# Kernel optimization log

Hardware: AMD Instinct MI355X
Metric: run time of the kernel (lower is better)

Reference implementation:

```python
import jax, jax.numpy as jnp
import numpy as np

SEQ, D_IN, D_OUT = 4096, 1024, 1024


def setup_inputs() -> dict:
    key = jax.random.key(0)
    kx, kq, kk, kv = jax.random.split(key, 4)
    x = jax.random.normal(kx, (SEQ, D_IN), dtype=jnp.float32)
    # original uses torch.rand (uniform [0,1)) for parameter init
    W_query = jax.random.uniform(kq, (D_IN, D_OUT), dtype=jnp.float32)
    W_key = jax.random.uniform(kk, (D_IN, D_OUT), dtype=jnp.float32)
    W_value = jax.random.uniform(kv, (D_IN, D_OUT), dtype=jnp.float32)
    return {"x": x, "W_query": W_query, "W_key": W_key, "W_value": W_value}


def reference(x, W_query, W_key, W_value):
    queries = x @ W_query          # [S, d_out]
    keys = x @ W_key               # [S, d_out]
    values = x @ W_value           # [S, d_out]
    scale = keys.shape[-1] ** 0.5
    attn_scores = queries @ keys.T # [S, S]
    attn_weights = jax.nn.softmax(attn_scores / scale, axis=-1)
    context_vec = attn_weights @ values  # [S, d_out]
    return context_vec
```

## Files before the change

### kernel.cpp

```cpp
#include <hip/hip_runtime.h>
#include <stdint.h>

#define SEQ 4096
#define DM 1024

typedef __attribute__((ext_vector_type(8))) short short8;
typedef __attribute__((ext_vector_type(4))) float f32x4;
typedef __attribute__((ext_vector_type(16))) float f32x16;
typedef unsigned short ushort_t;

__device__ inline ushort_t f2bf(float f) {
  union { float f; uint32_t u; } v; v.f = f;
  return (ushort_t)((v.u + 0x7FFFu + ((v.u >> 16) & 1u)) >> 16);
}
__device__ inline float bf2f(ushort_t h) {
  union { uint32_t u; float f; } v; v.u = ((uint32_t)h) << 16;
  return v.f;
}

__device__ inline void async_copy16(const void* g, void* lds) {
  __builtin_amdgcn_global_load_lds(
      (const __attribute__((address_space(1))) uint32_t*)g,
      (__attribute__((address_space(3))) uint32_t*)lds, 16, 0, 0);
}


__global__ __launch_bounds__(256, 3)
void gemm_qkv(const ushort_t* __restrict__ A, const ushort_t* __restrict__ Bt,
              ushort_t* __restrict__ Qb, ushort_t* __restrict__ Kb,
              ushort_t* __restrict__ Vb) {
  __shared__ ushort_t As[2][128 * 32];
  __shared__ ushort_t Bs[2][128 * 32];
  const int t = threadIdx.x;
  const int wave = t >> 6, lane = t & 63;
  const int quad = lane >> 4, l16 = lane & 15;
  const int m0 = blockIdx.y * 128, n0 = blockIdx.x * 128;
  const int wm = (wave & 1) * 64, wn = (wave >> 1) * 64;

  f32x4 acc[4][4] = {};

  if (n0 >= 2048) {
    ushort_t* Af = &As[0][0];
    ushort_t* Bf = &Bs[0][0];
    const int srow8 = lane >> 3;
    const int gcol8 = (((lane & 7) - srow8) & 7) * 8;
    const int rs = l16 & 7;
    for (int k0 = 0; k0 < 1024; k0 += 64) {
#pragma unroll
      for (int i = 0; i < 4; ++i) {
        int c = wave * 4 + i;
        async_copy16(A + (size_t)(m0 + c * 8 + srow8) * 2048 + k0 + gcol8,
                     Af + c * 512);
        async_copy16(Bt + (size_t)(n0 + c * 8 + srow8) * 2048 + k0 + gcol8,
                     Bf + c * 512);
      }
      __syncthreads();
#pragma unroll
      for (int q = 0; q < 2; ++q) {
        short8 a[4], b[4];
#pragma unroll
        for (int i = 0; i < 4; ++i) {
          int slot = ((q * 4 + quad + rs) & 7) * 8;
          a[i] = *(const short8*)(Af + (wm + i * 16 + l16) * 64 + slot);
          b[i] = *(const short8*)(Bf + (wn + i * 16 + l16) * 64 + slot);
        }
#pragma unroll
        for (int i = 0; i < 4; ++i)
#pragma unroll
          for (int j = 0; j < 4; ++j)
            acc[i][j] = __builtin_amdgcn_mfma_f32_16x16x32_bf16(a[i], b[j], acc[i][j], 0, 0, 0);
      }
      __syncthreads();
    }
    const int cb = n0 - 2048;
#pragma unroll
    for (int i = 0; i < 4; ++i)
#pragma unroll
      for (int j = 0; j < 4; ++j)
#pragma unroll
        for (int r = 0; r < 4; ++r) {
          int row = m0 + wm + i * 16 + quad * 4 + r;
          int col = cb + wn + j * 16 + l16;
          Vb[(size_t)row * 1024 + col] = f2bf(acc[i][j][r]);
        }
    return;
  }

  const int srow = lane >> 2;
  const int sf = (srow >> 1) & 3;
  const int gcol = (((lane & 3) - sf) & 3) * 8;
  const int rf = (l16 >> 1) & 3;
  const int aslot = ((quad + rf) & 3) * 8;

  for (int k0 = 0; k0 < 1024; k0 += 32) {
#pragma unroll
    for (int i = 0; i < 2; ++i) {
      int c = wave * 2 + i;
      const ushort_t* ga = A + (size_t)(m0 + c * 16 + srow) * 2048 + k0 + gcol;
      const ushort_t* gb = Bt + (size_t)(n0 + c * 16 + srow) * 2048 + k0 + gcol;
      async_copy16(ga,        As[0] + c * 512);
      async_copy16(ga + 1024, As[1] + c * 512);
      async_copy16(gb,        Bs[0] + c * 512);
      async_copy16(gb + 1024, Bs[1] + c * 512);
    }
    __syncthreads();
    short8 a[4], b[4], x[4];
#pragma unroll
    for (int i = 0; i < 4; ++i) {
      a[i] = *(const short8*)(As[0] + (wm + i * 16 + l16) * 32 + aslot);
      b[i] = *(const short8*)(Bs[0] + (wn + i * 16 + l16) * 32 + aslot);
    }
#pragma unroll
    for (int i = 0; i < 4; ++i)
#pragma unroll
      for (int j = 0; j < 4; ++j)
        acc[i][j] = __builtin_amdgcn_mfma_f32_16x16x32_bf16(a[i], b[j], acc[i][j], 0, 0, 0);
#pragma unroll
    for (int j = 0; j < 4; ++j)
      x[j] = *(const short8*)(Bs[1] + (wn + j * 16 + l16) * 32 + aslot);
#pragma unroll
    for (int i = 0; i < 4; ++i)
#pragma unroll
      for (int j = 0; j < 4; ++j)
        acc[i][j] = __builtin_amdgcn_mfma_f32_16x16x32_bf16(a[i], x[j], acc[i][j], 0, 0, 0);
#pragma unroll
    for (int i = 0; i < 4; ++i)
      x[i] = *(const short8*)(As[1] + (wm + i * 16 + l16) * 32 + aslot);
#pragma unroll
    for (int i = 0; i < 4; ++i)
#pragma unroll
      for (int j = 0; j < 4; ++j)
        acc[i][j] = __builtin_amdgcn_mfma_f32_16x16x32_bf16(x[i], b[j], acc[i][j], 0, 0, 0);
    __syncthreads();
  }

  ushort_t* Cm = (n0 < 1024) ? Qb : Kb;
  const int cb = n0 & 1023;
#pragma unroll
  for (int i = 0; i < 4; ++i)
#pragma unroll
    for (int j = 0; j < 4; ++j)
#pragma unroll
      for (int r = 0; r < 4; ++r) {
        int row = m0 + wm + i * 16 + quad * 4 + r;
        int col = cb + wn + j * 16 + l16;
        float v = acc[i][j][r];
        ushort_t h = f2bf(v);
        size_t base = (size_t)row * 2048 + col;
        Cm[base] = h;
        Cm[base + 1024] = f2bf(v - bf2f(h));
      }
}

__global__ __launch_bounds__(256, 4)
void gemm_sc(const ushort_t* __restrict__ A, const ushort_t* __restrict__ Bt,
             float* __restrict__ C, float scale) {
  const int m0 = blockIdx.y * 128, n0 = blockIdx.x * 128;

  __shared__ ushort_t As[2][128 * 32];
  __shared__ ushort_t Bs[2][128 * 32];
  const int t = threadIdx.x;
  const int wave = t >> 6, lane = t & 63;
  const int quad = lane >> 4, l16 = lane & 15;
  const int wm = (wave & 1) * 64, wn = (wave >> 1) * 64;
  const int srow = lane >> 2;
  const int sf = (srow >> 1) & 3;
  const int gcol = (((lane & 3) - sf) & 3) * 8;
  const int rf = (l16 >> 1) & 3;
  const int aslot = ((quad + rf) & 3) * 8;

  f32x4 acc[4][4] = {};

  for (int k0 = 0; k0 < 1024; k0 += 32) {
#pragma unroll
    for (int i = 0; i < 2; ++i) {
      int c = wave * 2 + i;
      const ushort_t* ga = A + (size_t)(m0 + c * 16 + srow) * 2048 + k0 + gcol;
      const ushort_t* gb = Bt + (size_t)(n0 + c * 16 + srow) * 2048 + k0 + gcol;
      async_copy16(ga,        As[0] + c * 512);
      async_copy16(ga + 1024, As[1] + c * 512);
      async_copy16(gb,        Bs[0] + c * 512);
      async_copy16(gb + 1024, Bs[1] + c * 512);
    }
    __syncthreads();
    short8 a[4], b[4], x[4];
#pragma unroll
    for (int i = 0; i < 4; ++i) {
      a[i] = *(const short8*)(As[0] + (wm + i * 16 + l16) * 32 + aslot);
      b[i] = *(const short8*)(Bs[0] + (wn + i * 16 + l16) * 32 + aslot);
    }
#pragma unroll
    for (int i = 0; i < 4; ++i)
#pragma unroll
      for (int j = 0; j < 4; ++j)
        acc[i][j] = __builtin_amdgcn_mfma_f32_16x16x32_bf16(a[i], b[j], acc[i][j], 0, 0, 0);
#pragma unroll
    for (int j = 0; j < 4; ++j)
      x[j] = *(const short8*)(Bs[1] + (wn + j * 16 + l16) * 32 + aslot);
#pragma unroll
    for (int i = 0; i < 4; ++i)
#pragma unroll
      for (int j = 0; j < 4; ++j)
        acc[i][j] = __builtin_amdgcn_mfma_f32_16x16x32_bf16(a[i], x[j], acc[i][j], 0, 0, 0);
#pragma unroll
    for (int i = 0; i < 4; ++i)
      x[i] = *(const short8*)(As[1] + (wm + i * 16 + l16) * 32 + aslot);
#pragma unroll
    for (int i = 0; i < 4; ++i)
#pragma unroll
      for (int j = 0; j < 4; ++j)
        acc[i][j] = __builtin_amdgcn_mfma_f32_16x16x32_bf16(x[i], b[j], acc[i][j], 0, 0, 0);
    __syncthreads();
  }

#pragma unroll
  for (int i = 0; i < 4; ++i)
#pragma unroll
    for (int j = 0; j < 4; ++j)
#pragma unroll
      for (int r = 0; r < 4; ++r) {
        int row = m0 + wm + i * 16 + quad * 4 + r;
        int col = n0 + wn + j * 16 + l16;
        C[(size_t)row * SEQ + col] = acc[i][j][r] * scale;
      }
}

__global__ __launch_bounds__(256)
void gemm_pv(const ushort_t* __restrict__ P, const ushort_t* __restrict__ Vt,
             float* __restrict__ Obuf) {
  const int id = blockIdx.x;
  const int g = ((id >> 6) << 3) | (id & 7);
  const int jt = (id >> 3) & 7;
  const int z = g & 3, m = g >> 2;
  const int m0 = m * 128, n0 = jt * 128, kbeg = z * 1024;
  float* Ob = Obuf + (size_t)z * SEQ * DM;

  __shared__ ushort_t As[128 * 64];
  __shared__ ushort_t Bs[128 * 64];
  const int t = threadIdx.x;
  const int wave = t >> 6, lane = t & 63;
  const int l32 = lane & 31, khalf = lane >> 5;
  const int wm = (wave & 1) * 64, wn = (wave >> 1) * 64;
  const int srow = lane >> 3;
  const int gcol = (((lane & 7) - srow) & 7) * 8;
  const int rrot = lane & 7;

  f32x16 acc[2][2] = {};
  for (int k0 = kbeg; k0 < kbeg + 1024; k0 += 64) {
#pragma unroll
    for (int i = 0; i < 4; ++i) {
      int c = wave * 4 + i;
      async_copy16(P + (size_t)(m0 + c * 8 + srow) * 4096 + k0 + gcol,
                   As + c * 512);
      async_copy16(Vt + (size_t)(n0 + c * 8 + srow) * SEQ + k0 + gcol,
                   Bs + c * 512);
    }
    __syncthreads();
#pragma unroll
    for (int q = 0; q < 4; ++q) {
      const int slot = ((q * 2 + khalf + rrot) & 7) * 8;
      short8 a[2], b[2];
#pragma unroll
      for (int i = 0; i < 2; ++i) {
        a[i] = *(const short8*)(As + (wm + i * 32 + l32) * 64 + slot);
        b[i] = *(const short8*)(Bs + (wn + i * 32 + l32) * 64 + slot);
      }
#pragma unroll
      for (int i = 0; i < 2; ++i)
#pragma unroll
        for (int j = 0; j < 2; ++j)
          acc[i][j] = __builtin_amdgcn_mfma_f32_32x32x16_bf16(a[i], b[j], acc[i][j], 0, 0, 0);
    }
    __syncthreads();
  }
#pragma unroll
  for (int i = 0; i < 2; ++i)
#pragma unroll
    for (int j = 0; j < 2; ++j)
#pragma unroll
      for (int r = 0; r < 16; ++r) {
        int row = m0 + wm + i * 32 + (r & 3) + 8 * (r >> 2) + 4 * khalf;
        int col = n0 + wn + j * 32 + l32;
        Ob[(size_t)row * DM + col] = acc[i][j][r];
      }
}

__global__ __launch_bounds__(256)
void reduce4(const float* __restrict__ B, float* __restrict__ out) {
  const size_t i = ((size_t)blockIdx.x * 256 + threadIdx.x) * 4;
  const size_t n = (size_t)SEQ * DM;
  float4 s0 = *(const float4*)(B + i);
  float4 s1 = *(const float4*)(B + n + i);
  float4 s2 = *(const float4*)(B + 2 * n + i);
  float4 s3 = *(const float4*)(B + 3 * n + i);
  float4 o;
  o.x = s0.x + s1.x + s2.x + s3.x;
  o.y = s0.y + s1.y + s2.y + s3.y;
  o.z = s0.z + s1.z + s2.z + s3.z;
  o.w = s0.w + s1.w + s2.w + s3.w;
  *(float4*)(out + i) = o;
}

__global__ __launch_bounds__(256)
void split_x(const float* __restrict__ x, ushort_t* __restrict__ Xp) {
  int idx = (blockIdx.x * 256 + threadIdx.x) * 4;
  int r = idx >> 10, c = idx & 1023;
  float4 v = *(const float4*)(x + idx);
  ushort4 hi, lo;
  hi.x = f2bf(v.x); lo.x = f2bf(v.x - bf2f(hi.x));
  hi.y = f2bf(v.y); lo.y = f2bf(v.y - bf2f(hi.y));
  hi.z = f2bf(v.z); lo.z = f2bf(v.z - bf2f(hi.z));
  hi.w = f2bf(v.w); lo.w = f2bf(v.w - bf2f(hi.w));
  *(ushort4*)(Xp + (size_t)r * 2048 + c) = hi;
  *(ushort4*)(Xp + (size_t)r * 2048 + 1024 + c) = lo;
}

__global__ __launch_bounds__(256)
void splitT_w3(const float* __restrict__ W0, const float* __restrict__ W1,
               const float* __restrict__ W2, ushort_t* __restrict__ Wp) {
  const float* W = (blockIdx.z == 0) ? W0 : (blockIdx.z == 1) ? W1 : W2;
  ushort_t* Wo = Wp + (size_t)blockIdx.z * DM * 2048;
  __shared__ float tile[64][65];
  const int bn = blockIdx.x * 64, bk = blockIdx.y * 64;
  const int tx = threadIdx.x & 63, ty = threadIdx.x >> 6;
#pragma unroll
  for (int i = ty; i < 64; i += 4)
    tile[i][tx] = W[(size_t)(bk + i) * DM + bn + tx];
  __syncthreads();
#pragma unroll
  for (int i = ty; i < 64; i += 4) {
    float v = tile[tx][i];
    ushort_t h = f2bf(v);
    Wo[(size_t)(bn + i) * 2048 + bk + tx] = h;
    Wo[(size_t)(bn + i) * 2048 + 1024 + bk + tx] = f2bf(v - bf2f(h));
  }
}

__global__ __launch_bounds__(256)
void transpose_bf16(const ushort_t* __restrict__ in, int istride,
                    ushort_t* __restrict__ out, int R) {
  __shared__ ushort_t tile[64][65];
  const int bc = blockIdx.x * 64, br = blockIdx.y * 64;
  const int tx = threadIdx.x & 63, ty = threadIdx.x >> 6;
#pragma unroll
  for (int i = ty; i < 64; i += 4)
    tile[i][tx] = in[(size_t)(br + i) * istride + bc + tx];
  __syncthreads();
#pragma unroll
  for (int i = ty; i < 64; i += 4)
    out[(size_t)(bc + i) * R + br + tx] = tile[tx][i];
}

__global__ __launch_bounds__(256)
void softmax_rows(const float* __restrict__ S, ushort_t* __restrict__ Pd) {
  const int row = blockIdx.x;
  const int t = threadIdx.x, lane = t & 63, wave = t >> 6;
  const float4* s4 = (const float4*)(S + (size_t)row * SEQ);
  float4 v[4];
  float m = -3.4e38f;
#pragma unroll
  for (int i = 0; i < 4; ++i) {
    v[i] = s4[i * 256 + t];
    m = fmaxf(m, fmaxf(fmaxf(v[i].x, v[i].y), fmaxf(v[i].z, v[i].w)));
  }
  __shared__ float redm[4], reds[4];
#pragma unroll
  for (int o = 32; o; o >>= 1) m = fmaxf(m, __shfl_xor(m, o));
  if (lane == 0) redm[wave] = m;
  __syncthreads();
  m = fmaxf(fmaxf(redm[0], redm[1]), fmaxf(redm[2], redm[3]));
  float sum = 0.f;
#pragma unroll
  for (int i = 0; i < 4; ++i) {
    v[i].x = __expf(v[i].x - m); v[i].y = __expf(v[i].y - m);
    v[i].z = __expf(v[i].z - m); v[i].w = __expf(v[i].w - m);
    sum += v[i].x + v[i].y + v[i].z + v[i].w;
  }
#pragma unroll
  for (int o = 32; o; o >>= 1) sum += __shfl_xor(sum, o);
  if (lane == 0) reds[wave] = sum;
  __syncthreads();
  const float inv = 1.f / (reds[0] + reds[1] + reds[2] + reds[3]);
  ushort4* p4 = (ushort4*)(Pd + (size_t)row * SEQ);
#pragma unroll
  for (int i = 0; i < 4; ++i) {
    ushort4 o;
    o.x = f2bf(v[i].x * inv); o.y = f2bf(v[i].y * inv);
    o.z = f2bf(v[i].z * inv); o.w = f2bf(v[i].w * inv);
    p4[i * 256 + t] = o;
  }
}

extern "C" void kernel_launch(void* const* d_in, const int* in_sizes, int n_in,
                              void* d_out, int out_size, void* d_ws, size_t ws_size,
                              hipStream_t stream) {
  const float* x  = (const float*)d_in[0];
  const float* Wq = (const float*)d_in[1];
  const float* Wk = (const float*)d_in[2];
  const float* Wv = (const float*)d_in[3];
  float* out = (float*)d_out;
  char* ws = (char*)d_ws;
  const size_t MB = (size_t)1 << 20;
  ushort_t* Xp   = (ushort_t*)(ws + 0 * MB);
  ushort_t* Wall = (ushort_t*)(ws + 16 * MB);
  ushort_t* Qb   = (ushort_t*)(ws + 28 * MB);
  ushort_t* Kb   = (ushort_t*)(ws + 44 * MB);
  ushort_t* Vb   = (ushort_t*)(ws + 60 * MB);
  ushort_t* VT   = (ushort_t*)(ws + 68 * MB);
  float*    S    = (float*)(ws + 76 * MB);
  ushort_t* Pd   = (ushort_t*)(ws + 0 * MB);
  float*    Obuf = (float*)(ws + 76 * MB);

  split_x<<<SEQ * DM / 1024, 256, 0, stream>>>(x, Xp);
  splitT_w3<<<dim3(16, 16, 3), 256, 0, stream>>>(Wq, Wk, Wv, Wall);

  gemm_qkv<<<dim3(3 * DM / 128, SEQ / 128), 256, 0, stream>>>(
      Xp, Wall, Qb, Kb, Vb);

  transpose_bf16<<<dim3(DM / 64, SEQ / 64), 256, 0, stream>>>(Vb, 1024, VT, SEQ);

  gemm_sc<<<dim3(SEQ / 128, SEQ / 128), 256, 0, stream>>>(Qb, Kb, S, 0.03125f);

  softmax_rows<<<SEQ, 256, 0, stream>>>(S, Pd);

  gemm_pv<<<1024, 256, 0, stream>>>(Pd, VT, Obuf);

  reduce4<<<SEQ * DM / 1024, 256, 0, stream>>>(Obuf, out);
}
```

Baseline: 320.8 us.

## Fuse V transpose into QKV epilogue, merge prep kernels, shrink PV tiles

```diff
diff --git a/kernel.cpp b/kernel.cpp
--- a/kernel.cpp
+++ b/kernel.cpp
@@ -28,7 +28,7 @@
 __global__ __launch_bounds__(256, 3)
 void gemm_qkv(const ushort_t* __restrict__ A, const ushort_t* __restrict__ Bt,
               ushort_t* __restrict__ Qb, ushort_t* __restrict__ Kb,
-              ushort_t* __restrict__ Vb) {
+              ushort_t* __restrict__ VT) {
   __shared__ ushort_t As[2][128 * 32];
   __shared__ ushort_t Bs[2][128 * 32];
   const int t = threadIdx.x;
@@ -76,13 +76,14 @@
 #pragma unroll
     for (int i = 0; i < 4; ++i)
 #pragma unroll
-      for (int j = 0; j < 4; ++j)
-#pragma unroll
-        for (int r = 0; r < 4; ++r) {
-          int row = m0 + wm + i * 16 + quad * 4 + r;
-          int col = cb + wn + j * 16 + l16;
-          Vb[(size_t)row * 1024 + col] = f2bf(acc[i][j][r]);
-        }
+      for (int j = 0; j < 4; ++j) {
+        int row_base = m0 + wm + i * 16 + quad * 4;
+        int col = cb + wn + j * 16 + l16;
+        ushort4 o;
+        o.x = f2bf(acc[i][j][0]); o.y = f2bf(acc[i][j][1]);
+        o.z = f2bf(acc[i][j][2]); o.w = f2bf(acc[i][j][3]);
+        *(ushort4*)(VT + (size_t)col * SEQ + row_base) = o;
+      }
     return;
   }
 
@@ -229,29 +230,33 @@
 void gemm_pv(const ushort_t* __restrict__ P, const ushort_t* __restrict__ Vt,
              float* __restrict__ Obuf) {
   const int id = blockIdx.x;
-  const int g = ((id >> 6) << 3) | (id & 7);
-  const int jt = (id >> 3) & 7;
+  const int g = ((id >> 7) << 3) | (id & 7);
+  const int jn = (id >> 3) & 15;
   const int z = g & 3, m = g >> 2;
-  const int m0 = m * 128, n0 = jt * 128, kbeg = z * 1024;
+  const int m0 = m * 128, n0 = jn * 64, kbeg = z * 1024;
   float* Ob = Obuf + (size_t)z * SEQ * DM;
 
   __shared__ ushort_t As[128 * 64];
-  __shared__ ushort_t Bs[128 * 64];
+  __shared__ ushort_t Bs[64 * 64];
   const int t = threadIdx.x;
   const int wave = t >> 6, lane = t & 63;
   const int l32 = lane & 31, khalf = lane >> 5;
-  const int wm = (wave & 1) * 64, wn = (wave >> 1) * 64;
+  const int wm = (wave & 1) * 64, wn = (wave >> 1) * 32;
   const int srow = lane >> 3;
   const int gcol = (((lane & 7) - srow) & 7) * 8;
   const int rrot = lane & 7;
 
-  f32x16 acc[2][2] = {};
+  f32x16 acc[2] = {};
   for (int k0 = kbeg; k0 < kbeg + 1024; k0 += 64) {
 #pragma unroll
     for (int i = 0; i < 4; ++i) {
       int c = wave * 4 + i;
       async_copy16(P + (size_t)(m0 + c * 8 + srow) * 4096 + k0 + gcol,
                    As + c * 512);
+    }
+#pragma unroll
+    for (int i = 0; i < 2; ++i) {
+      int c = wave * 2 + i;
       async_copy16(Vt + (size_t)(n0 + c * 8 + srow) * SEQ + k0 + gcol,
                    Bs + c * 512);
     }
@@ -259,30 +264,23 @@
 #pragma unroll
     for (int q = 0; q < 4; ++q) {
       const int slot = ((q * 2 + khalf + rrot) & 7) * 8;
-      short8 a[2], b[2];
+      short8 b = *(const short8*)(Bs + (wn + l32) * 64 + slot);
 #pragma unroll
       for (int i = 0; i < 2; ++i) {
-        a[i] = *(const short8*)(As + (wm + i * 32 + l32) * 64 + slot);
-        b[i] = *(const short8*)(Bs + (wn + i * 32 + l32) * 64 + slot);
-      }
-#pragma unroll
-      for (int i = 0; i < 2; ++i)
-#pragma unroll
-        for (int j = 0; j < 2; ++j)
-          acc[i][j] = __builtin_amdgcn_mfma_f32_32x32x16_bf16(a[i], b[j], acc[i][j], 0, 0, 0);
+        short8 a = *(const short8*)(As + (wm + i * 32 + l32) * 64 + slot);
+        acc[i] = __builtin_amdgcn_mfma_f32_32x32x16_bf16(a, b, acc[i], 0, 0, 0);
+      }
     }
     __syncthreads();
   }
 #pragma unroll
   for (int i = 0; i < 2; ++i)
 #pragma unroll
-    for (int j = 0; j < 2; ++j)
-#pragma unroll
-      for (int r = 0; r < 16; ++r) {
-        int row = m0 + wm + i * 32 + (r & 3) + 8 * (r >> 2) + 4 * khalf;
-        int col = n0 + wn + j * 32 + l32;
-        Ob[(size_t)row * DM + col] = acc[i][j][r];
-      }
+    for (int r = 0; r < 16; ++r) {
+      int row = m0 + wm + i * 32 + (r & 3) + 8 * (r >> 2) + 4 * khalf;
+      int col = n0 + wn + l32;
+      Ob[(size_t)row * DM + col] = acc[i][r];
+    }
 }
 
 __global__ __launch_bounds__(256)
@@ -302,27 +300,27 @@
 }
 
 __global__ __launch_bounds__(256)
-void split_x(const float* __restrict__ x, ushort_t* __restrict__ Xp) {
-  int idx = (blockIdx.x * 256 + threadIdx.x) * 4;
-  int r = idx >> 10, c = idx & 1023;
-  float4 v = *(const float4*)(x + idx);
-  ushort4 hi, lo;
-  hi.x = f2bf(v.x); lo.x = f2bf(v.x - bf2f(hi.x));
-  hi.y = f2bf(v.y); lo.y = f2bf(v.y - bf2f(hi.y));
-  hi.z = f2bf(v.z); lo.z = f2bf(v.z - bf2f(hi.z));
-  hi.w = f2bf(v.w); lo.w = f2bf(v.w - bf2f(hi.w));
-  *(ushort4*)(Xp + (size_t)r * 2048 + c) = hi;
-  *(ushort4*)(Xp + (size_t)r * 2048 + 1024 + c) = lo;
-}
-
-__global__ __launch_bounds__(256)
-void splitT_w3(const float* __restrict__ W0, const float* __restrict__ W1,
-               const float* __restrict__ W2, ushort_t* __restrict__ Wp) {
-  const float* W = (blockIdx.z == 0) ? W0 : (blockIdx.z == 1) ? W1 : W2;
-  ushort_t* Wo = Wp + (size_t)blockIdx.z * DM * 2048;
+void prep(const float* __restrict__ x, const float* __restrict__ W0,
+          const float* __restrict__ W1, const float* __restrict__ W2,
+          ushort_t* __restrict__ Xp, ushort_t* __restrict__ Wall) {
+  const int zz = blockIdx.z;
+  const int tx = threadIdx.x & 63, ty = threadIdx.x >> 6;
+  if (zz == 3) {
+    const int bc = blockIdx.x * 64, br = blockIdx.y * 64;
+#pragma unroll
+    for (int i = ty; i < 64; i += 4) {
+      float v = x[(size_t)(br + i) * 1024 + bc + tx];
+      ushort_t h = f2bf(v);
+      Xp[(size_t)(br + i) * 2048 + bc + tx] = h;
+      Xp[(size_t)(br + i) * 2048 + 1024 + bc + tx] = f2bf(v - bf2f(h));
+    }
+    return;
+  }
+  if (blockIdx.y >= 16) return;
+  const float* W = (zz == 0) ? W0 : (zz == 1) ? W1 : W2;
+  ushort_t* Wo = Wall + (size_t)zz * DM * 2048;
   __shared__ float tile[64][65];
   const int bn = blockIdx.x * 64, bk = blockIdx.y * 64;
-  const int tx = threadIdx.x & 63, ty = threadIdx.x >> 6;
 #pragma unroll
   for (int i = ty; i < 64; i += 4)
     tile[i][tx] = W[(size_t)(bk + i) * DM + bn + tx];
@@ -334,21 +332,6 @@
     Wo[(size_t)(bn + i) * 2048 + bk + tx] = h;
     Wo[(size_t)(bn + i) * 2048 + 1024 + bk + tx] = f2bf(v - bf2f(h));
   }
-}
-
-__global__ __launch_bounds__(256)
-void transpose_bf16(const ushort_t* __restrict__ in, int istride,
-                    ushort_t* __restrict__ out, int R) {
-  __shared__ ushort_t tile[64][65];
-  const int bc = blockIdx.x * 64, br = blockIdx.y * 64;
-  const int tx = threadIdx.x & 63, ty = threadIdx.x >> 6;
-#pragma unroll
-  for (int i = ty; i < 64; i += 4)
-    tile[i][tx] = in[(size_t)(br + i) * istride + bc + tx];
-  __syncthreads();
-#pragma unroll
-  for (int i = ty; i < 64; i += 4)
-    out[(size_t)(bc + i) * R + br + tx] = tile[tx][i];
 }
 
 __global__ __launch_bounds__(256)
@@ -405,25 +388,21 @@
   ushort_t* Wall = (ushort_t*)(ws + 16 * MB);
   ushort_t* Qb   = (ushort_t*)(ws + 28 * MB);
   ushort_t* Kb   = (ushort_t*)(ws + 44 * MB);
-  ushort_t* Vb   = (ushort_t*)(ws + 60 * MB);
   ushort_t* VT   = (ushort_t*)(ws + 68 * MB);
   float*    S    = (float*)(ws + 76 * MB);
   ushort_t* Pd   = (ushort_t*)(ws + 0 * MB);
   float*    Obuf = (float*)(ws + 76 * MB);
 
-  split_x<<<SEQ * DM / 1024, 256, 0, stream>>>(x, Xp);
-  splitT_w3<<<dim3(16, 16, 3), 256, 0, stream>>>(Wq, Wk, Wv, Wall);
+  prep<<<dim3(16, 64, 4), 256, 0, stream>>>(x, Wq, Wk, Wv, Xp, Wall);
 
   gemm_qkv<<<dim3(3 * DM / 128, SEQ / 128), 256, 0, stream>>>(
-      Xp, Wall, Qb, Kb, Vb);
-
-  transpose_bf16<<<dim3(DM / 64, SEQ / 64), 256, 0, stream>>>(Vb, 1024, VT, SEQ);
+      Xp, Wall, Qb, Kb, VT);
 
   gemm_sc<<<dim3(SEQ / 128, SEQ / 128), 256, 0, stream>>>(Qb, Kb, S, 0.03125f);
 
   softmax_rows<<<SEQ, 256, 0, stream>>>(S, Pd);
 
-  gemm_pv<<<1024, 256, 0, stream>>>(Pd, VT, Obuf);
+  gemm_pv<<<2048, 256, 0, stream>>>(Pd, VT, Obuf);
 
   reduce4<<<SEQ * DM / 1024, 256, 0, stream>>>(Obuf, out);
 }
```

Result: faster. 301.6 us (-6.0%).
